# Kernel optimization log

Hardware: AMD Instinct MI355X
Metric: run time of the kernel (lower is better)

The kernel has to match this reference:

```python
import jax, jax.numpy as jnp
import numpy as np

B, Z, C, H = 4096, 128, 12, 512


def setup_inputs() -> dict:
    key = jax.random.key(0)
    ks = jax.random.split(key, 9)
    obs = jax.random.normal(ks[0], (B, Z, C), dtype=jnp.float32)
    action_count = jax.random.uniform(ks[1], (B, Z, Z), dtype=jnp.float32)
    adj_mask = jax.random.randint(ks[2], (Z, Z), 0, 2, dtype=jnp.int32)
    travel_times = jax.random.randint(ks[3], (Z, Z), 0, C, dtype=jnp.int32)
    w0 = jax.random.uniform(ks[4], (1,), dtype=jnp.float32)
    W1 = jax.random.normal(ks[5], (Z, H), dtype=jnp.float32) / np.sqrt(Z).astype(np.float32)
    b1 = jnp.zeros((H,), dtype=jnp.float32)
    W2 = jax.random.normal(ks[6], (H, H), dtype=jnp.float32) / np.sqrt(H).astype(np.float32)
    b2 = jnp.zeros((H,), dtype=jnp.float32)
    Wf = jax.random.normal(ks[7], (H, 1), dtype=jnp.float32) / np.sqrt(H).astype(np.float32)
    bf = jnp.zeros((1,), dtype=jnp.float32)
    return {"obs": obs, "action_count": action_count, "w0": w0,
            "W1": W1, "b1": b1, "W2": W2, "b2": b2, "Wf": Wf, "bf": bf,
            "adj_mask": adj_mask, "travel_times": travel_times}


def reference(obs, action_count, w0, W1, b1, W2, b2, Wf, bf, adj_mask, travel_times):
    # temporal decay weights: w[c] = exp(-w0 * c), c in [0, C)
    w = jnp.exp(-w0[0] * jnp.arange(C, dtype=jnp.float32))  # [C]
    # Fused equivalent of the per-zone loops:
    # temp[b,i,c] = obs[b,i,c] + sum_{j in adj(i), tt[j,i]==c} action_count[b,j,i]
    # next[b,i]   = sum_c temp[b,i,c] * w[c]
    #             = obs[b,i,:].w + sum_j adj[j,i]*w[tt[j,i]]*action_count[b,j,i]
    M = adj_mask.astype(jnp.float32) * w[travel_times]  # [Z, Z] edge weights j->i
    next_state_count = jnp.einsum('bic,c->bi', obs, w) + jnp.einsum('bji,ji->bi', action_count, M)
    # small MLP head
    x = jax.nn.relu(next_state_count @ W1 + b1)
    x = jax.nn.relu(x @ W2 + b2)
    symbolic_val = (x @ Wf + bf)[:, 0]  # [B]
    return symbolic_val, next_state_count
```

## Files before the change

kernel.cpp:

```cpp
#include <hip/hip_runtime.h>
#include <math.h>

#define ZZ 128
#define CC 12
#define HH 512
#define NB 4096

typedef __attribute__((ext_vector_type(8))) short short8;
typedef __attribute__((ext_vector_type(4))) float f32x4;

__device__ __forceinline__ unsigned short f2bf(float x) {
    unsigned u = __builtin_bit_cast(unsigned, x);
    u += 0x7FFFu + ((u >> 16) & 1u);
    return (unsigned short)(u >> 16);
}
__device__ __forceinline__ float bf2f(unsigned short h) {
    unsigned u = ((unsigned)h) << 16;
    return __builtin_bit_cast(float, u);
}

__global__ __launch_bounds__(256) void k_prep(const float* __restrict__ W1,
                                              const float* __restrict__ W2,
                                              const int* __restrict__ adj,
                                              const int* __restrict__ tt,
                                              const float* __restrict__ w0p,
                                              const float* __restrict__ bfp,
                                              short* __restrict__ W1tH, short* __restrict__ W1tL,
                                              short* __restrict__ W2tH, short* __restrict__ W2tL,
                                              float* __restrict__ M, float* __restrict__ outv) {
    int bid = blockIdx.x, t = threadIdx.x;
    if (bid < 80) {
        __shared__ float T[64][65];
        const float* src; short *dH, *dL; int k0, n0, Krows;
        if (bid < 64) { src = W2; dH = W2tH; dL = W2tL; Krows = HH; k0 = (bid & 7) * 64; n0 = (bid >> 3) * 64; }
        else { int b = bid - 64; src = W1; dH = W1tH; dL = W1tL; Krows = ZZ; k0 = (b & 1) * 64; n0 = (b >> 1) * 64; }
#pragma unroll
        for (int it = 0; it < 16; ++it) {
            int idx = t + it * 256; int r = idx >> 6, c = idx & 63;
            T[r][c] = src[(size_t)(k0 + r) * HH + n0 + c];
        }
        __syncthreads();
#pragma unroll
        for (int it = 0; it < 16; ++it) {
            int idx = t + it * 256; int nl = idx >> 6, kl = idx & 63;
            float v = T[kl][nl];
            unsigned short h = f2bf(v);
            float lo = v - bf2f(h);
            size_t o = (size_t)(n0 + nl) * Krows + k0 + kl;
            dH[o] = (short)h; dL[o] = (short)f2bf(lo);
        }
    } else if (bid == 80) {
        float w0 = w0p[0];
#pragma unroll
        for (int it = 0; it < 64; ++it) {
            int e = t + it * 256;
            M[e] = adj[e] ? expf(-w0 * (float)tt[e]) : 0.f;
        }
    } else {
        float bv = bfp[0];
#pragma unroll
        for (int it = 0; it < 16; ++it) outv[t + it * 256] = bv;
    }
}

__global__ __launch_bounds__(256) void k_next(const float* __restrict__ obs,
                                              const float* __restrict__ act,
                                              const float* __restrict__ M,
                                              const float* __restrict__ w0p,
                                              float* __restrict__ outn,
                                              short* __restrict__ nxtH,
                                              short* __restrict__ nxtL) {
    __shared__ float P[2][4][128];
    __shared__ float wsh[16];
    int t = threadIdx.x;
    int b0 = blockIdx.x * 2;
    if (t < CC) wsh[t] = expf(-w0p[0] * (float)t);
    int i4 = t & 31, jg = (t >> 5) & 3, bo = t >> 7;
    const float* abase = act + (size_t)(b0 + bo) * ZZ * ZZ;
    float4 acc = make_float4(0.f, 0.f, 0.f, 0.f);
#pragma unroll 8
    for (int jj = 0; jj < 32; ++jj) {
        int j = jg * 32 + jj;
        float4 a = *(const float4*)&abase[j * ZZ + i4 * 4];
        float4 m = *(const float4*)&M[j * ZZ + i4 * 4];
        acc.x += a.x * m.x; acc.y += a.y * m.y; acc.z += a.z * m.z; acc.w += a.w * m.w;
    }
    *(float4*)&P[bo][jg][i4 * 4] = acc;
    __syncthreads();
    int i = t & 127, bo2 = t >> 7;
    int bb = b0 + bo2;
    float s = P[bo2][0][i] + P[bo2][1][i] + P[bo2][2][i] + P[bo2][3][i];
    const float* orow = obs + ((size_t)bb * ZZ + i) * CC;
#pragma unroll
    for (int c = 0; c < CC; ++c) s += orow[c] * wsh[c];
    outn[(size_t)bb * ZZ + i] = s;
    unsigned short h = f2bf(s);
    nxtH[bb * ZZ + i] = (short)h;
    nxtL[bb * ZZ + i] = (short)f2bf(s - bf2f(h));
}

#define GBM 64
#define GBN 128
#define GBK 64

__global__ __launch_bounds__(128) void k_gemm(const short* __restrict__ Ah,
                                              const short* __restrict__ Al,
                                              const short* __restrict__ Bh,
                                              const short* __restrict__ Bl,
                                              const float* __restrict__ bias,
                                              int Kdim, int mode,
                                              short* __restrict__ OutH,
                                              short* __restrict__ OutL,
                                              const float* __restrict__ Wf,
                                              float* __restrict__ OutDot) {
    __shared__ __align__(16) short AsH[GBM * GBK], AsL[GBM * GBK];
    __shared__ __align__(16) short BsH[GBN * GBK], BsL[GBN * GBK];
    int t = threadIdx.x;
    int m0 = blockIdx.y * GBM, n0 = blockIdx.x * GBN;
    int lane = t & 63, wn = t >> 6;
    int l15 = lane & 15, l4 = lane >> 4;
    f32x4 acc[4][4] = {};

    for (int k0 = 0; k0 < Kdim; k0 += GBK) {
#pragma unroll
        for (int it = 0; it < 4; ++it) {
            int idx = t + it * 128; int row = idx >> 3, ch = idx & 7, cs = ch ^ (row & 7);
            *(int4*)&AsH[row * GBK + cs * 8] = *(const int4*)&Ah[(size_t)(m0 + row) * Kdim + k0 + ch * 8];
            *(int4*)&AsL[row * GBK + cs * 8] = *(const int4*)&Al[(size_t)(m0 + row) * Kdim + k0 + ch * 8];
        }
#pragma unroll
        for (int it = 0; it < 8; ++it) {
            int idx = t + it * 128; int row = idx >> 3, ch = idx & 7, cs = ch ^ (row & 7);
            *(int4*)&BsH[row * GBK + cs * 8] = *(const int4*)&Bh[(size_t)(n0 + row) * Kdim + k0 + ch * 8];
            *(int4*)&BsL[row * GBK + cs * 8] = *(const int4*)&Bl[(size_t)(n0 + row) * Kdim + k0 + ch * 8];
        }
        __syncthreads();
#pragma unroll
        for (int s = 0; s < 2; ++s) {
            short8 ah[4], al[4], bh[4], bl[4];
            int g = s * 4 + l4;
#pragma unroll
            for (int mf = 0; mf < 4; ++mf) {
                int row = mf * 16 + l15;
                int addr = row * GBK + ((g ^ (row & 7)) << 3);
                ah[mf] = *(const short8*)&AsH[addr];
                al[mf] = *(const short8*)&AsL[addr];
            }
#pragma unroll
            for (int nf = 0; nf < 4; ++nf) {
                int row = wn * 64 + nf * 16 + l15;
                int addr = row * GBK + ((g ^ (row & 7)) << 3);
                bh[nf] = *(const short8*)&BsH[addr];
                bl[nf] = *(const short8*)&BsL[addr];
            }
#pragma unroll
            for (int mf = 0; mf < 4; ++mf)
#pragma unroll
                for (int nf = 0; nf < 4; ++nf) {
                    acc[mf][nf] = __builtin_amdgcn_mfma_f32_16x16x32_bf16(ah[mf], bh[nf], acc[mf][nf], 0, 0, 0);
                    acc[mf][nf] = __builtin_amdgcn_mfma_f32_16x16x32_bf16(ah[mf], bl[nf], acc[mf][nf], 0, 0, 0);
                    acc[mf][nf] = __builtin_amdgcn_mfma_f32_16x16x32_bf16(al[mf], bh[nf], acc[mf][nf], 0, 0, 0);
                }
        }
        __syncthreads();
    }

    if (mode == 0) {
#pragma unroll
        for (int mf = 0; mf < 4; ++mf)
#pragma unroll
            for (int nf = 0; nf < 4; ++nf) {
                int col = n0 + wn * 64 + nf * 16 + l15;
                float bv = bias[col];
#pragma unroll
                for (int r = 0; r < 4; ++r) {
                    int row = m0 + mf * 16 + l4 * 4 + r;
                    float v = fmaxf(acc[mf][nf][r] + bv, 0.f);
                    unsigned short h = f2bf(v);
                    OutH[(size_t)row * HH + col] = (short)h;
                    OutL[(size_t)row * HH + col] = (short)f2bf(v - bf2f(h));
                }
            }
    } else {
        float bv[4], wv[4];
#pragma unroll
        for (int nf = 0; nf < 4; ++nf) {
            int col = n0 + wn * 64 + nf * 16 + l15;
            bv[nf] = bias[col];
            wv[nf] = Wf[col];
        }
#pragma unroll
        for (int mf = 0; mf < 4; ++mf)
#pragma unroll
            for (int r = 0; r < 4; ++r) {
                float p = 0.f;
#pragma unroll
                for (int nf = 0; nf < 4; ++nf)
                    p += fmaxf(acc[mf][nf][r] + bv[nf], 0.f) * wv[nf];
                p += __shfl_xor(p, 1);
                p += __shfl_xor(p, 2);
                p += __shfl_xor(p, 4);
                p += __shfl_xor(p, 8);
                if (l15 == 0) {
                    int row = m0 + mf * 16 + l4 * 4 + r;
                    atomicAdd(&OutDot[row], p);
                }
            }
    }
}

extern "C" void kernel_launch(void* const* d_in, const int* in_sizes, int n_in,
                              void* d_out, int out_size, void* d_ws, size_t ws_size,
                              hipStream_t stream) {
    const float* obs = (const float*)d_in[0];
    const float* act = (const float*)d_in[1];
    const float* w0  = (const float*)d_in[2];
    const float* W1  = (const float*)d_in[3];
    const float* b1  = (const float*)d_in[4];
    const float* W2  = (const float*)d_in[5];
    const float* b2  = (const float*)d_in[6];
    const float* Wf  = (const float*)d_in[7];
    const float* bf  = (const float*)d_in[8];
    const int* adj   = (const int*)d_in[9];
    const int* tt    = (const int*)d_in[10];

    float* out = (float*)d_out;
    float* outn = out + NB;

    char* base = (char*)d_ws;
    float* M    = (float*)base;
    short* nxtH = (short*)(base + (1u << 16));
    short* nxtL = (short*)(base + (1u << 16) + (1u << 20));
    char* p = base + (1u << 16) + (2u << 20);
    short* W1tH = (short*)p;               p += (size_t)HH * ZZ * 2;
    short* W1tL = (short*)p;               p += (size_t)HH * ZZ * 2;
    short* W2tH = (short*)p;               p += (size_t)HH * HH * 2;
    short* W2tL = (short*)p;               p += (size_t)HH * HH * 2;
    short* x1H  = (short*)p;               p += (size_t)NB * HH * 2;
    short* x1L  = (short*)p;

    k_prep<<<82, 256, 0, stream>>>(W1, W2, adj, tt, w0, bf,
                                   W1tH, W1tL, W2tH, W2tL, M, out);
    k_next<<<NB / 2, 256, 0, stream>>>(obs, act, M, w0, outn, nxtH, nxtL);

    dim3 g(HH / GBN, NB / GBM);
    k_gemm<<<g, 128, 0, stream>>>(nxtH, nxtL, W1tH, W1tL, b1, ZZ, 0,
                                  x1H, x1L, (const float*)nullptr, (float*)nullptr);
    k_gemm<<<g, 128, 0, stream>>>(x1H, x1L, W2tH, W2tL, b2, HH, 1,
                                  (short*)nullptr, (short*)nullptr, Wf, out);
}
```

Before: 138.7 us.

## Stage obs through shared memory and retile GEMM to 64x64 with four waves

```diff
diff --git a/kernel.cpp b/kernel.cpp
--- a/kernel.cpp
+++ b/kernel.cpp
@@ -71,10 +71,28 @@
                                               short* __restrict__ nxtH,
                                               short* __restrict__ nxtL) {
     __shared__ float P[2][4][128];
+    __shared__ float obsS[2][CC][128];
     __shared__ float wsh[16];
     int t = threadIdx.x;
     int b0 = blockIdx.x * 2;
-    if (t < CC) wsh[t] = expf(-w0p[0] * (float)t);
+    if (t < 16) wsh[t] = (t < CC) ? expf(-w0p[0] * (float)t) : 0.f;
+
+    const float4* og = (const float4*)(obs + (size_t)b0 * ZZ * CC);
+#pragma unroll
+    for (int it = 0; it < 3; ++it) {
+        int idx = t + it * 256;
+        float4 v = og[idx];
+        int e = idx * 4;
+        int bo = idx / 384;
+        int rem = e - bo * 1536;
+        int i = rem / CC;
+        int c = rem - i * CC;
+        obsS[bo][c + 0][i] = v.x;
+        obsS[bo][c + 1][i] = v.y;
+        obsS[bo][c + 2][i] = v.z;
+        obsS[bo][c + 3][i] = v.w;
+    }
+
     int i4 = t & 31, jg = (t >> 5) & 3, bo = t >> 7;
     const float* abase = act + (size_t)(b0 + bo) * ZZ * ZZ;
     float4 acc = make_float4(0.f, 0.f, 0.f, 0.f);
@@ -87,23 +105,21 @@
     }
     *(float4*)&P[bo][jg][i4 * 4] = acc;
     __syncthreads();
+
     int i = t & 127, bo2 = t >> 7;
     int bb = b0 + bo2;
     float s = P[bo2][0][i] + P[bo2][1][i] + P[bo2][2][i] + P[bo2][3][i];
-    const float* orow = obs + ((size_t)bb * ZZ + i) * CC;
-#pragma unroll
-    for (int c = 0; c < CC; ++c) s += orow[c] * wsh[c];
+#pragma unroll
+    for (int c = 0; c < CC; ++c) s += obsS[bo2][c][i] * wsh[c];
     outn[(size_t)bb * ZZ + i] = s;
     unsigned short h = f2bf(s);
     nxtH[bb * ZZ + i] = (short)h;
     nxtL[bb * ZZ + i] = (short)f2bf(s - bf2f(h));
 }
 
-#define GBM 64
-#define GBN 128
 #define GBK 64
 
-__global__ __launch_bounds__(128) void k_gemm(const short* __restrict__ Ah,
+__global__ __launch_bounds__(256) void k_gemm(const short* __restrict__ Ah,
                                               const short* __restrict__ Al,
                                               const short* __restrict__ Bh,
                                               const short* __restrict__ Bl,
@@ -113,50 +129,48 @@
                                               short* __restrict__ OutL,
                                               const float* __restrict__ Wf,
                                               float* __restrict__ OutDot) {
-    __shared__ __align__(16) short AsH[GBM * GBK], AsL[GBM * GBK];
-    __shared__ __align__(16) short BsH[GBN * GBK], BsL[GBN * GBK];
+    __shared__ __align__(16) short AsH[64 * GBK], AsL[64 * GBK];
+    __shared__ __align__(16) short BsH[64 * GBK], BsL[64 * GBK];
     int t = threadIdx.x;
-    int m0 = blockIdx.y * GBM, n0 = blockIdx.x * GBN;
-    int lane = t & 63, wn = t >> 6;
+    int m0 = blockIdx.y * 64, n0 = blockIdx.x * 64;
+    int lane = t & 63, w = t >> 6;
+    int wm = w >> 1, wn = w & 1;
     int l15 = lane & 15, l4 = lane >> 4;
-    f32x4 acc[4][4] = {};
+    f32x4 acc[2][2] = {};
 
     for (int k0 = 0; k0 < Kdim; k0 += GBK) {
 #pragma unroll
-        for (int it = 0; it < 4; ++it) {
-            int idx = t + it * 128; int row = idx >> 3, ch = idx & 7, cs = ch ^ (row & 7);
+        for (int it = 0; it < 2; ++it) {
+            int idx = t + it * 256;
+            int row = idx >> 3, ch = idx & 7, cs = ch ^ (row & 7);
             *(int4*)&AsH[row * GBK + cs * 8] = *(const int4*)&Ah[(size_t)(m0 + row) * Kdim + k0 + ch * 8];
             *(int4*)&AsL[row * GBK + cs * 8] = *(const int4*)&Al[(size_t)(m0 + row) * Kdim + k0 + ch * 8];
-        }
-#pragma unroll
-        for (int it = 0; it < 8; ++it) {
-            int idx = t + it * 128; int row = idx >> 3, ch = idx & 7, cs = ch ^ (row & 7);
             *(int4*)&BsH[row * GBK + cs * 8] = *(const int4*)&Bh[(size_t)(n0 + row) * Kdim + k0 + ch * 8];
             *(int4*)&BsL[row * GBK + cs * 8] = *(const int4*)&Bl[(size_t)(n0 + row) * Kdim + k0 + ch * 8];
         }
         __syncthreads();
 #pragma unroll
         for (int s = 0; s < 2; ++s) {
-            short8 ah[4], al[4], bh[4], bl[4];
             int g = s * 4 + l4;
-#pragma unroll
-            for (int mf = 0; mf < 4; ++mf) {
-                int row = mf * 16 + l15;
+            short8 ah[2], al[2], bh[2], bl[2];
+#pragma unroll
+            for (int mf = 0; mf < 2; ++mf) {
+                int row = wm * 32 + mf * 16 + l15;
                 int addr = row * GBK + ((g ^ (row & 7)) << 3);
                 ah[mf] = *(const short8*)&AsH[addr];
                 al[mf] = *(const short8*)&AsL[addr];
             }
 #pragma unroll
-            for (int nf = 0; nf < 4; ++nf) {
-                int row = wn * 64 + nf * 16 + l15;
+            for (int nf = 0; nf < 2; ++nf) {
+                int row = wn * 32 + nf * 16 + l15;
                 int addr = row * GBK + ((g ^ (row & 7)) << 3);
                 bh[nf] = *(const short8*)&BsH[addr];
                 bl[nf] = *(const short8*)&BsL[addr];
             }
 #pragma unroll
-            for (int mf = 0; mf < 4; ++mf)
-#pragma unroll
-                for (int nf = 0; nf < 4; ++nf) {
+            for (int mf = 0; mf < 2; ++mf)
+#pragma unroll
+                for (int nf = 0; nf < 2; ++nf) {
                     acc[mf][nf] = __builtin_amdgcn_mfma_f32_16x16x32_bf16(ah[mf], bh[nf], acc[mf][nf], 0, 0, 0);
                     acc[mf][nf] = __builtin_amdgcn_mfma_f32_16x16x32_bf16(ah[mf], bl[nf], acc[mf][nf], 0, 0, 0);
                     acc[mf][nf] = __builtin_amdgcn_mfma_f32_16x16x32_bf16(al[mf], bh[nf], acc[mf][nf], 0, 0, 0);
@@ -167,14 +181,14 @@
 
     if (mode == 0) {
 #pragma unroll
-        for (int mf = 0; mf < 4; ++mf)
-#pragma unroll
-            for (int nf = 0; nf < 4; ++nf) {
-                int col = n0 + wn * 64 + nf * 16 + l15;
+        for (int mf = 0; mf < 2; ++mf)
+#pragma unroll
+            for (int nf = 0; nf < 2; ++nf) {
+                int col = n0 + wn * 32 + nf * 16 + l15;
                 float bv = bias[col];
 #pragma unroll
                 for (int r = 0; r < 4; ++r) {
-                    int row = m0 + mf * 16 + l4 * 4 + r;
+                    int row = m0 + wm * 32 + mf * 16 + l4 * 4 + r;
                     float v = fmaxf(acc[mf][nf][r] + bv, 0.f);
                     unsigned short h = f2bf(v);
                     OutH[(size_t)row * HH + col] = (short)h;
@@ -182,27 +196,27 @@
                 }
             }
     } else {
-        float bv[4], wv[4];
-#pragma unroll
-        for (int nf = 0; nf < 4; ++nf) {
-            int col = n0 + wn * 64 + nf * 16 + l15;
+        float bv[2], wv[2];
+#pragma unroll
+        for (int nf = 0; nf < 2; ++nf) {
+            int col = n0 + wn * 32 + nf * 16 + l15;
             bv[nf] = bias[col];
             wv[nf] = Wf[col];
         }
 #pragma unroll
-        for (int mf = 0; mf < 4; ++mf)
+        for (int mf = 0; mf < 2; ++mf)
 #pragma unroll
             for (int r = 0; r < 4; ++r) {
                 float p = 0.f;
 #pragma unroll
-                for (int nf = 0; nf < 4; ++nf)
+                for (int nf = 0; nf < 2; ++nf)
                     p += fmaxf(acc[mf][nf][r] + bv[nf], 0.f) * wv[nf];
                 p += __shfl_xor(p, 1);
                 p += __shfl_xor(p, 2);
                 p += __shfl_xor(p, 4);
                 p += __shfl_xor(p, 8);
                 if (l15 == 0) {
-                    int row = m0 + mf * 16 + l4 * 4 + r;
+                    int row = m0 + wm * 32 + mf * 16 + l4 * 4 + r;
                     atomicAdd(&OutDot[row], p);
                 }
             }
@@ -243,9 +257,9 @@
                                    W1tH, W1tL, W2tH, W2tL, M, out);
     k_next<<<NB / 2, 256, 0, stream>>>(obs, act, M, w0, outn, nxtH, nxtL);
 
-    dim3 g(HH / GBN, NB / GBM);
-    k_gemm<<<g, 128, 0, stream>>>(nxtH, nxtL, W1tH, W1tL, b1, ZZ, 0,
+    dim3 g(HH / 64, NB / 64);
+    k_gemm<<<g, 256, 0, stream>>>(nxtH, nxtL, W1tH, W1tL, b1, ZZ, 0,
                                   x1H, x1L, (const float*)nullptr, (float*)nullptr);
-    k_gemm<<<g, 128, 0, stream>>>(x1H, x1L, W2tH, W2tL, b2, HH, 1,
+    k_gemm<<<g, 256, 0, stream>>>(x1H, x1L, W2tH, W2tL, b2, HH, 1,
                                   (short*)nullptr, (short*)nullptr, Wf, out);
 }
```

After: 130.0 us. 6.3% less time.

## Fuse next-state computation and both MLP layers into one per-row-block kernel

Applied to the files above, without the earlier changes.

```diff
diff --git a/kernel.cpp b/kernel.cpp
--- a/kernel.cpp
+++ b/kernel.cpp
@@ -5,6 +5,8 @@
 #define CC 12
 #define HH 512
 #define NB 4096
+#define RPB 16
+#define NBLK (NB / RPB)
 
 typedef __attribute__((ext_vector_type(8))) short short8;
 typedef __attribute__((ext_vector_type(4))) float f32x4;
@@ -24,10 +26,9 @@
                                               const int* __restrict__ adj,
                                               const int* __restrict__ tt,
                                               const float* __restrict__ w0p,
-                                              const float* __restrict__ bfp,
                                               short* __restrict__ W1tH, short* __restrict__ W1tL,
                                               short* __restrict__ W2tH, short* __restrict__ W2tL,
-                                              float* __restrict__ M, float* __restrict__ outv) {
+                                              float* __restrict__ M) {
     int bid = blockIdx.x, t = threadIdx.x;
     if (bid < 80) {
         __shared__ float T[64][65];
@@ -49,164 +50,178 @@
             size_t o = (size_t)(n0 + nl) * Krows + k0 + kl;
             dH[o] = (short)h; dL[o] = (short)f2bf(lo);
         }
-    } else if (bid == 80) {
+    } else {
         float w0 = w0p[0];
 #pragma unroll
         for (int it = 0; it < 64; ++it) {
             int e = t + it * 256;
             M[e] = adj[e] ? expf(-w0 * (float)tt[e]) : 0.f;
         }
-    } else {
-        float bv = bfp[0];
-#pragma unroll
-        for (int it = 0; it < 16; ++it) outv[t + it * 256] = bv;
-    }
-}
-
-__global__ __launch_bounds__(256) void k_next(const float* __restrict__ obs,
-                                              const float* __restrict__ act,
-                                              const float* __restrict__ M,
-                                              const float* __restrict__ w0p,
-                                              float* __restrict__ outn,
-                                              short* __restrict__ nxtH,
-                                              short* __restrict__ nxtL) {
-    __shared__ float P[2][4][128];
-    __shared__ float wsh[16];
+    }
+}
+
+__global__ __launch_bounds__(256) void k_fused(const float* __restrict__ obs,
+                                               const float* __restrict__ act,
+                                               const float* __restrict__ M,
+                                               const float* __restrict__ w0p,
+                                               const short* __restrict__ W1tH,
+                                               const short* __restrict__ W1tL,
+                                               const short* __restrict__ W2tH,
+                                               const short* __restrict__ W2tL,
+                                               const float* __restrict__ b1,
+                                               const float* __restrict__ b2,
+                                               const float* __restrict__ Wf,
+                                               const float* __restrict__ bfp,
+                                               float* __restrict__ out) {
+    __shared__ __align__(16) short AsH[RPB * ZZ], AsL[RPB * ZZ];
+    __shared__ __align__(16) short X1H[RPB * HH], X1L[RPB * HH];
+    __shared__ float red[4][RPB];
+
     int t = threadIdx.x;
-    int b0 = blockIdx.x * 2;
-    if (t < CC) wsh[t] = expf(-w0p[0] * (float)t);
-    int i4 = t & 31, jg = (t >> 5) & 3, bo = t >> 7;
-    const float* abase = act + (size_t)(b0 + bo) * ZZ * ZZ;
-    float4 acc = make_float4(0.f, 0.f, 0.f, 0.f);
-#pragma unroll 8
-    for (int jj = 0; jj < 32; ++jj) {
-        int j = jg * 32 + jj;
-        float4 a = *(const float4*)&abase[j * ZZ + i4 * 4];
-        float4 m = *(const float4*)&M[j * ZZ + i4 * 4];
-        acc.x += a.x * m.x; acc.y += a.y * m.y; acc.z += a.z * m.z; acc.w += a.w * m.w;
-    }
-    *(float4*)&P[bo][jg][i4 * 4] = acc;
+    int b0 = blockIdx.x * RPB;
+    int b_loc = t >> 4, ig = t & 15;
+
+    const float* ab = act + (size_t)(b0 + b_loc) * ZZ * ZZ + ig * 8;
+    const float* mb = M + ig * 8;
+    float4 na = make_float4(0.f, 0.f, 0.f, 0.f);
+    float4 nb = make_float4(0.f, 0.f, 0.f, 0.f);
+#pragma unroll 4
+    for (int j = 0; j < ZZ; ++j) {
+        float4 a0 = *(const float4*)(ab + (size_t)j * ZZ);
+        float4 a1 = *(const float4*)(ab + (size_t)j * ZZ + 4);
+        float4 m0 = *(const float4*)(mb + j * ZZ);
+        float4 m1 = *(const float4*)(mb + j * ZZ + 4);
+        na.x += a0.x * m0.x; na.y += a0.y * m0.y; na.z += a0.z * m0.z; na.w += a0.w * m0.w;
+        nb.x += a1.x * m1.x; nb.y += a1.y * m1.y; nb.z += a1.z * m1.z; nb.w += a1.w * m1.w;
+    }
+    float w[CC];
+    {
+        float e = expf(-w0p[0]);
+        w[0] = 1.f;
+#pragma unroll
+        for (int c = 1; c < CC; ++c) w[c] = w[c - 1] * e;
+    }
+    float nx[8] = {na.x, na.y, na.z, na.w, nb.x, nb.y, nb.z, nb.w};
+    const float* ob = obs + ((size_t)(b0 + b_loc) * ZZ + ig * 8) * CC;
+#pragma unroll
+    for (int r = 0; r < 8; ++r) {
+        float4 o0 = *(const float4*)(ob + r * CC);
+        float4 o1 = *(const float4*)(ob + r * CC + 4);
+        float4 o2 = *(const float4*)(ob + r * CC + 8);
+        nx[r] += o0.x * w[0] + o0.y * w[1] + o0.z * w[2] + o0.w * w[3]
+               + o1.x * w[4] + o1.y * w[5] + o1.z * w[6] + o1.w * w[7]
+               + o2.x * w[8] + o2.y * w[9] + o2.z * w[10] + o2.w * w[11];
+    }
+    float* on = out + NB + (size_t)(b0 + b_loc) * ZZ + ig * 8;
+    *(float4*)on = make_float4(nx[0], nx[1], nx[2], nx[3]);
+    *(float4*)(on + 4) = make_float4(nx[4], nx[5], nx[6], nx[7]);
+    {
+        int row = b_loc;
+        int cs = (ig ^ (row & 7)) << 3;
+        short8 hi, lo;
+#pragma unroll
+        for (int r = 0; r < 8; ++r) {
+            unsigned short h = f2bf(nx[r]);
+            hi[r] = (short)h;
+            lo[r] = (short)f2bf(nx[r] - bf2f(h));
+        }
+        *(short8*)&AsH[row * ZZ + cs] = hi;
+        *(short8*)&AsL[row * ZZ + cs] = lo;
+    }
     __syncthreads();
-    int i = t & 127, bo2 = t >> 7;
-    int bb = b0 + bo2;
-    float s = P[bo2][0][i] + P[bo2][1][i] + P[bo2][2][i] + P[bo2][3][i];
-    const float* orow = obs + ((size_t)bb * ZZ + i) * CC;
-#pragma unroll
-    for (int c = 0; c < CC; ++c) s += orow[c] * wsh[c];
-    outn[(size_t)bb * ZZ + i] = s;
-    unsigned short h = f2bf(s);
-    nxtH[bb * ZZ + i] = (short)h;
-    nxtL[bb * ZZ + i] = (short)f2bf(s - bf2f(h));
-}
-
-#define GBM 64
-#define GBN 128
-#define GBK 64
-
-__global__ __launch_bounds__(128) void k_gemm(const short* __restrict__ Ah,
-                                              const short* __restrict__ Al,
-                                              const short* __restrict__ Bh,
-                                              const short* __restrict__ Bl,
-                                              const float* __restrict__ bias,
-                                              int Kdim, int mode,
-                                              short* __restrict__ OutH,
-                                              short* __restrict__ OutL,
-                                              const float* __restrict__ Wf,
-                                              float* __restrict__ OutDot) {
-    __shared__ __align__(16) short AsH[GBM * GBK], AsL[GBM * GBK];
-    __shared__ __align__(16) short BsH[GBN * GBK], BsL[GBN * GBK];
-    int t = threadIdx.x;
-    int m0 = blockIdx.y * GBM, n0 = blockIdx.x * GBN;
-    int lane = t & 63, wn = t >> 6;
+
+    int lane = t & 63, wv = t >> 6;
     int l15 = lane & 15, l4 = lane >> 4;
-    f32x4 acc[4][4] = {};
-
-    for (int k0 = 0; k0 < Kdim; k0 += GBK) {
-#pragma unroll
-        for (int it = 0; it < 4; ++it) {
-            int idx = t + it * 128; int row = idx >> 3, ch = idx & 7, cs = ch ^ (row & 7);
-            *(int4*)&AsH[row * GBK + cs * 8] = *(const int4*)&Ah[(size_t)(m0 + row) * Kdim + k0 + ch * 8];
-            *(int4*)&AsL[row * GBK + cs * 8] = *(const int4*)&Al[(size_t)(m0 + row) * Kdim + k0 + ch * 8];
-        }
-#pragma unroll
-        for (int it = 0; it < 8; ++it) {
-            int idx = t + it * 128; int row = idx >> 3, ch = idx & 7, cs = ch ^ (row & 7);
-            *(int4*)&BsH[row * GBK + cs * 8] = *(const int4*)&Bh[(size_t)(n0 + row) * Kdim + k0 + ch * 8];
-            *(int4*)&BsL[row * GBK + cs * 8] = *(const int4*)&Bl[(size_t)(n0 + row) * Kdim + k0 + ch * 8];
-        }
-        __syncthreads();
-#pragma unroll
-        for (int s = 0; s < 2; ++s) {
-            short8 ah[4], al[4], bh[4], bl[4];
-            int g = s * 4 + l4;
-#pragma unroll
-            for (int mf = 0; mf < 4; ++mf) {
-                int row = mf * 16 + l15;
-                int addr = row * GBK + ((g ^ (row & 7)) << 3);
-                ah[mf] = *(const short8*)&AsH[addr];
-                al[mf] = *(const short8*)&AsL[addr];
-            }
-#pragma unroll
-            for (int nf = 0; nf < 4; ++nf) {
-                int row = wn * 64 + nf * 16 + l15;
-                int addr = row * GBK + ((g ^ (row & 7)) << 3);
-                bh[nf] = *(const short8*)&BsH[addr];
-                bl[nf] = *(const short8*)&BsL[addr];
-            }
-#pragma unroll
-            for (int mf = 0; mf < 4; ++mf)
-#pragma unroll
-                for (int nf = 0; nf < 4; ++nf) {
-                    acc[mf][nf] = __builtin_amdgcn_mfma_f32_16x16x32_bf16(ah[mf], bh[nf], acc[mf][nf], 0, 0, 0);
-                    acc[mf][nf] = __builtin_amdgcn_mfma_f32_16x16x32_bf16(ah[mf], bl[nf], acc[mf][nf], 0, 0, 0);
-                    acc[mf][nf] = __builtin_amdgcn_mfma_f32_16x16x32_bf16(al[mf], bh[nf], acc[mf][nf], 0, 0, 0);
-                }
-        }
-        __syncthreads();
-    }
-
-    if (mode == 0) {
-#pragma unroll
-        for (int mf = 0; mf < 4; ++mf)
-#pragma unroll
-            for (int nf = 0; nf < 4; ++nf) {
-                int col = n0 + wn * 64 + nf * 16 + l15;
-                float bv = bias[col];
-#pragma unroll
-                for (int r = 0; r < 4; ++r) {
-                    int row = m0 + mf * 16 + l4 * 4 + r;
-                    float v = fmaxf(acc[mf][nf][r] + bv, 0.f);
-                    unsigned short h = f2bf(v);
-                    OutH[(size_t)row * HH + col] = (short)h;
-                    OutL[(size_t)row * HH + col] = (short)f2bf(v - bf2f(h));
-                }
-            }
-    } else {
-        float bv[4], wv[4];
-#pragma unroll
-        for (int nf = 0; nf < 4; ++nf) {
-            int col = n0 + wn * 64 + nf * 16 + l15;
-            bv[nf] = bias[col];
-            wv[nf] = Wf[col];
-        }
-#pragma unroll
-        for (int mf = 0; mf < 4; ++mf)
-#pragma unroll
-            for (int r = 0; r < 4; ++r) {
-                float p = 0.f;
-#pragma unroll
-                for (int nf = 0; nf < 4; ++nf)
-                    p += fmaxf(acc[mf][nf][r] + bv[nf], 0.f) * wv[nf];
-                p += __shfl_xor(p, 1);
-                p += __shfl_xor(p, 2);
-                p += __shfl_xor(p, 4);
-                p += __shfl_xor(p, 8);
-                if (l15 == 0) {
-                    int row = m0 + mf * 16 + l4 * 4 + r;
-                    atomicAdd(&OutDot[row], p);
-                }
-            }
-    }
+    int nwb = wv * 128;
+    f32x4 acc[8] = {};
+    float b1c[8];
+#pragma unroll
+    for (int nf = 0; nf < 8; ++nf) b1c[nf] = b1[nwb + nf * 16 + l15];
+#pragma unroll
+    for (int s = 0; s < 4; ++s) {
+        int chunk = s * 4 + l4;
+        int aaddr = l15 * ZZ + ((chunk ^ (l15 & 7)) << 3);
+        short8 ah = *(const short8*)&AsH[aaddr];
+        short8 al = *(const short8*)&AsL[aaddr];
+        short8 bh[8], bl[8];
+#pragma unroll
+        for (int nf = 0; nf < 8; ++nf) {
+            int n = nwb + nf * 16 + l15;
+            bh[nf] = *(const short8*)&W1tH[(size_t)n * ZZ + chunk * 8];
+            bl[nf] = *(const short8*)&W1tL[(size_t)n * ZZ + chunk * 8];
+        }
+#pragma unroll
+        for (int nf = 0; nf < 8; ++nf) {
+            acc[nf] = __builtin_amdgcn_mfma_f32_16x16x32_bf16(ah, bh[nf], acc[nf], 0, 0, 0);
+            acc[nf] = __builtin_amdgcn_mfma_f32_16x16x32_bf16(ah, bl[nf], acc[nf], 0, 0, 0);
+            acc[nf] = __builtin_amdgcn_mfma_f32_16x16x32_bf16(al, bh[nf], acc[nf], 0, 0, 0);
+        }
+    }
+#pragma unroll
+    for (int nf = 0; nf < 8; ++nf) {
+        int col = nwb + nf * 16 + l15;
+        int chunk2 = col >> 3, cw = col & 7;
+#pragma unroll
+        for (int r = 0; r < 4; ++r) {
+            int row = l4 * 4 + r;
+            float v = fmaxf(acc[nf][r] + b1c[nf], 0.f);
+            unsigned short h = f2bf(v);
+            int addr = row * HH + ((chunk2 ^ (row & 7)) << 3) + cw;
+            X1H[addr] = (short)h;
+            X1L[addr] = (short)f2bf(v - bf2f(h));
+        }
+    }
+    __syncthreads();
+
+    f32x4 acc2[8] = {};
+#pragma unroll 2
+    for (int ks = 0; ks < 16; ++ks) {
+        int chunk = ks * 4 + l4;
+        int aaddr = l15 * HH + ((chunk ^ (l15 & 7)) << 3);
+        short8 ah = *(const short8*)&X1H[aaddr];
+        short8 al = *(const short8*)&X1L[aaddr];
+        short8 bh[8], bl[8];
+#pragma unroll
+        for (int nf = 0; nf < 8; ++nf) {
+            int n = nwb + nf * 16 + l15;
+            bh[nf] = *(const short8*)&W2tH[(size_t)n * HH + chunk * 8];
+            bl[nf] = *(const short8*)&W2tL[(size_t)n * HH + chunk * 8];
+        }
+#pragma unroll
+        for (int nf = 0; nf < 8; ++nf) {
+            acc2[nf] = __builtin_amdgcn_mfma_f32_16x16x32_bf16(ah, bh[nf], acc2[nf], 0, 0, 0);
+            acc2[nf] = __builtin_amdgcn_mfma_f32_16x16x32_bf16(ah, bl[nf], acc2[nf], 0, 0, 0);
+            acc2[nf] = __builtin_amdgcn_mfma_f32_16x16x32_bf16(al, bh[nf], acc2[nf], 0, 0, 0);
+        }
+    }
+
+    float b2c[8], wfc[8];
+#pragma unroll
+    for (int nf = 0; nf < 8; ++nf) {
+        int col = nwb + nf * 16 + l15;
+        b2c[nf] = b2[col];
+        wfc[nf] = Wf[col];
+    }
+    float p[4];
+#pragma unroll
+    for (int r = 0; r < 4; ++r) {
+        float s = 0.f;
+#pragma unroll
+        for (int nf = 0; nf < 8; ++nf)
+            s += fmaxf(acc2[nf][r] + b2c[nf], 0.f) * wfc[nf];
+        s += __shfl_xor(s, 1);
+        s += __shfl_xor(s, 2);
+        s += __shfl_xor(s, 4);
+        s += __shfl_xor(s, 8);
+        p[r] = s;
+    }
+    if (l15 == 0) {
+#pragma unroll
+        for (int r = 0; r < 4; ++r) red[wv][l4 * 4 + r] = p[r];
+    }
+    __syncthreads();
+    if (t < RPB)
+        out[b0 + t] = red[0][t] + red[1][t] + red[2][t] + red[3][t] + bfp[0];
 }
 
 extern "C" void kernel_launch(void* const* d_in, const int* in_sizes, int n_in,
@@ -225,27 +240,16 @@
     const int* tt    = (const int*)d_in[10];
 
     float* out = (float*)d_out;
-    float* outn = out + NB;
 
     char* base = (char*)d_ws;
     float* M    = (float*)base;
-    short* nxtH = (short*)(base + (1u << 16));
-    short* nxtL = (short*)(base + (1u << 16) + (1u << 20));
-    char* p = base + (1u << 16) + (2u << 20);
-    short* W1tH = (short*)p;               p += (size_t)HH * ZZ * 2;
-    short* W1tL = (short*)p;               p += (size_t)HH * ZZ * 2;
-    short* W2tH = (short*)p;               p += (size_t)HH * HH * 2;
-    short* W2tL = (short*)p;               p += (size_t)HH * HH * 2;
-    short* x1H  = (short*)p;               p += (size_t)NB * HH * 2;
-    short* x1L  = (short*)p;
-
-    k_prep<<<82, 256, 0, stream>>>(W1, W2, adj, tt, w0, bf,
-                                   W1tH, W1tL, W2tH, W2tL, M, out);
-    k_next<<<NB / 2, 256, 0, stream>>>(obs, act, M, w0, outn, nxtH, nxtL);
-
-    dim3 g(HH / GBN, NB / GBM);
-    k_gemm<<<g, 128, 0, stream>>>(nxtH, nxtL, W1tH, W1tL, b1, ZZ, 0,
-                                  x1H, x1L, (const float*)nullptr, (float*)nullptr);
-    k_gemm<<<g, 128, 0, stream>>>(x1H, x1L, W2tH, W2tL, b2, HH, 1,
-                                  (short*)nullptr, (short*)nullptr, Wf, out);
-}
+    char* p = base + (1u << 16);
+    short* W1tH = (short*)p;  p += (size_t)HH * ZZ * 2;
+    short* W1tL = (short*)p;  p += (size_t)HH * ZZ * 2;
+    short* W2tH = (short*)p;  p += (size_t)HH * HH * 2;
+    short* W2tL = (short*)p;
+
+    k_prep<<<81, 256, 0, stream>>>(W1, W2, adj, tt, w0, W1tH, W1tL, W2tH, W2tL, M);
+    k_fused<<<NBLK, 256, 0, stream>>>(obs, act, M, w0, W1tH, W1tL, W2tH, W2tL,
+                                      b1, b2, Wf, bf, out);
+}
```

Measured after the change: 153.9 us. 10.9% more time.
